# Kernel tuning notes

Measured on AMD Instinct MI355X. Metric: run time of the kernel, lower is better.

Reference implementation:

```python
import jax, jax.numpy as jnp
import numpy as np

PATCH, STRIDE, TOPK, EPS = 16, 8, 8, 1e-8

def _leaky(x):
    return jax.nn.leaky_relu(x, 0.01)

def setup_inputs() -> dict:
    key = jax.random.key(0)
    ks = jax.random.split(key, 12)
    s = 0.05  # small weight scale to avoid tanh saturation
    return {
        "X":      jax.random.normal(ks[0], (16, 4096, 512), jnp.float32),
        "W_enc1": jax.random.normal(ks[1], (512, 256), jnp.float32) * s,
        "b_enc1": jax.random.normal(ks[2], (256,), jnp.float32) * s,
        "W_enc2": jax.random.normal(ks[3], (256, 64), jnp.float32) * s,
        "b_enc2": jax.random.normal(ks[4], (64,), jnp.float32) * s,
        "Wq":     jax.random.normal(ks[5], (64, 64), jnp.float32) * s,
        "Wk":     jax.random.normal(ks[6], (64, 64), jnp.float32) * s,
        "Wv":     jax.random.normal(ks[7], (64, 64), jnp.float32) * s,
        "W_agg":  jax.random.normal(ks[8], (64, 64), jnp.float32) * s,
        "b_agg":  jax.random.normal(ks[9], (64,), jnp.float32) * s,
        "W_dec":  jax.random.normal(ks[10], (64, 512), jnp.float32) * s,
        "b_dec":  jax.random.normal(ks[11], (512,), jnp.float32) * s,
    }

def reference(X, W_enc1, b_enc1, W_enc2, b_enc2, Wq, Wk, Wv, W_agg, b_agg, W_dec, b_dec):
    B, L, D = X.shape
    # var_encoder (dropout-free MLP)
    Xe = _leaky(X @ W_enc1 + b_enc1) @ W_enc2 + b_enc2          # (B, L, d)
    d = Xe.shape[-1]
    # unfold into overlapping patches
    h = (L - PATCH) // STRIDE + 1
    pos = jnp.arange(h)[:, None] * STRIDE + jnp.arange(PATCH)[None, :]  # (h, PATCH)
    patches = Xe[:, pos, :]                                      # (B, h, PATCH, d)
    per_patch = patches.mean(axis=2).reshape(B * h, d)           # (N, d)
    q = per_patch @ Wq
    k = per_patch @ Wk
    v = per_patch @ Wv                                           # (N, hqk)
    qn = q / (jnp.linalg.norm(q, axis=-1, keepdims=True) + EPS)
    kn = k / (jnp.linalg.norm(k, axis=-1, keepdims=True) + EPS)
    # antisymmetric outer product, (N, hqk, hqk)
    M = qn[:, :, None] * kn[:, None, :] - kn[:, :, None] * qn[:, None, :]
    A = jax.nn.relu(jnp.tanh(M))
    n = A.shape[-1]
    # topk pruning along last dim via scatter-style mask
    _, idx = jax.lax.top_k(A, TOPK)                              # (N, n, TOPK)
    mask = jnp.any(idx[..., None] == jnp.arange(n), axis=-2)     # (N, n, n) bool
    A = A * mask.astype(A.dtype)
    A = A / jnp.maximum(A.sum(axis=-1, keepdims=True), EPS)
    Av = jnp.einsum('nij,nj->ni', A, v)                          # (N, hqk)
    # after_agg (dropout = identity in eval)
    z = _leaky(Av @ W_agg + b_agg)                               # (N, d)
    zB = z.reshape(B, h, d)
    # overlap-add fold: each patch writes its (constant-over-time) z to its window
    seg = jnp.broadcast_to(zB[:, :, None, :], (B, h, PATCH, d)).reshape(B, h * PATCH, d)
    flat_pos = pos.reshape(-1)                                   # (h*PATCH,)
    out = jnp.zeros((B, L, d), X.dtype).at[:, flat_pos, :].add(seg)
    counts = jnp.zeros((L,), X.dtype).at[flat_pos].add(1.0)
    out = out / jnp.maximum(counts, 1.0)[None, :, None]
    return out @ W_dec + b_dec                                   # (B, L, D)
```

## Files before the change

### kernel.cpp

```cpp
#include <hip/hip_runtime.h>


typedef __attribute__((ext_vector_type(8))) _Float16 half8;
typedef __attribute__((ext_vector_type(4))) _Float16 half4;
typedef __attribute__((ext_vector_type(4))) float floatx4;

__device__ __forceinline__ _Float16 f2h(float f) { return (_Float16)f; }

#define MFMA16(A, B, C) __builtin_amdgcn_mfma_f32_16x16x32_f16((A), (B), (C), 0, 0, 0)

__global__ __launch_bounds__(256) void prep_weights(
    const float* __restrict__ W1, const float* __restrict__ W2,
    const float* __restrict__ Wd,
    _Float16* __restrict__ W1t, _Float16* __restrict__ W2t,
    _Float16* __restrict__ Wdt)
{
    int idx = blockIdx.x * 256 + threadIdx.x;
    { int n = idx >> 9, k = idx & 511;  W1t[idx] = f2h(W1[k * 256 + n]); }
    if (idx < 16384) { int n = idx >> 8, k = idx & 255; W2t[idx] = f2h(W2[k * 64 + n]); }
    if (idx < 32768) { int n = idx >> 6, k = idx & 63;  Wdt[idx] = f2h(Wd[k * 512 + n]); }
}

__global__ __launch_bounds__(256) void enc_fused(
    const float* __restrict__ X, const _Float16* __restrict__ W1t,
    const float* __restrict__ b1, const _Float16* __restrict__ W2t,
    const float* __restrict__ b2, float* __restrict__ Gs)
{
    __shared__ _Float16 smem[20992];
    _Float16* As   = smem;
    _Float16* Bs   = smem + 4608;
    _Float16* Hs16 = smem;

    const int tid  = threadIdx.x;
    const int lane = tid & 63;
    const int w    = tid >> 6;
    const int m0   = blockIdx.x * 64;

    const int arow  = tid >> 2;
    const int akseg = (tid & 3) << 4;
    const float* Abase = X + (size_t)(m0 + arow) * 512 + akseg;

    const int brow0  = (w << 6) + (lane >> 3);
    const int bchunk = (((lane & 7) ^ ((lane >> 3) & 7)) << 3);

    floatx4 acc1[4][4];
#pragma unroll
    for (int ci = 0; ci < 4; ci++)
#pragma unroll
        for (int mi = 0; mi < 4; mi++) acc1[ci][mi] = (floatx4){0.f, 0.f, 0.f, 0.f};

    float4 pa[4];
    auto loadA = [&](int kt) {
#pragma unroll
        for (int u = 0; u < 4; u++) pa[u] = *(const float4*)(Abase + kt + 4 * u);
    };

    loadA(0);
    for (int kt = 0; kt < 512; kt += 64) {
#pragma unroll
        for (int inst = 0; inst < 8; inst++) {
            const _Float16* src = W1t + (size_t)(brow0 + inst * 8) * 512 + kt + bchunk;
            __builtin_amdgcn_global_load_lds(
                (const __attribute__((address_space(1))) unsigned int*)src,
                (__attribute__((address_space(3))) unsigned int*)(Bs + ((w << 6) + inst * 8) * 64),
                16, 0, 0);
        }
        {
            _Float16* d = &As[arow * 72 + akseg];
#pragma unroll
            for (int h = 0; h < 2; h++) {
                float4 f0 = pa[2 * h], f1 = pa[2 * h + 1];
                half8 o;
                o[0] = f2h(f0.x); o[1] = f2h(f0.y); o[2] = f2h(f0.z); o[3] = f2h(f0.w);
                o[4] = f2h(f1.x); o[5] = f2h(f1.y); o[6] = f2h(f1.z); o[7] = f2h(f1.w);
                *(half8*)(d + 8 * h) = o;
            }
        }
        __syncthreads();
        if (kt + 64 < 512) loadA(kt + 64);
#pragma unroll
        for (int ks = 0; ks < 2; ks++) {
            const int lchunk = ks * 4 + (lane >> 4);
            half8 af[4], bf[4];
#pragma unroll
            for (int ci = 0; ci < 4; ci++) {
                const int c = (w << 6) + ci * 16 + (lane & 15);
                af[ci] = *(const half8*)&Bs[c * 64 + ((lchunk ^ (lane & 7)) << 3)];
            }
#pragma unroll
            for (int mi = 0; mi < 4; mi++)
                bf[mi] = *(const half8*)&As[(mi * 16 + (lane & 15)) * 72 + ks * 32 + ((lane >> 4) << 3)];
#pragma unroll
            for (int ci = 0; ci < 4; ci++)
#pragma unroll
                for (int mi = 0; mi < 4; mi++)
                    acc1[ci][mi] = MFMA16(af[ci], bf[mi], acc1[ci][mi]);
        }
        __syncthreads();
    }

    float4 b1v[4];
#pragma unroll
    for (int ci = 0; ci < 4; ci++)
        b1v[ci] = *(const float4*)&b1[(w << 6) + ci * 16 + ((lane >> 4) << 2)];
#pragma unroll
    for (int ci = 0; ci < 4; ci++) {
#pragma unroll
        for (int mi = 0; mi < 4; mi++) {
            float vs[4];
#pragma unroll
            for (int r = 0; r < 4; r++) {
                float v = acc1[ci][mi][r] + ((const float*)&b1v[ci])[r];
                vs[r] = v > 0.f ? v : 0.01f * v;
            }
#pragma unroll
            for (int r = 0; r < 4; r++) {
                vs[r] += __shfl_xor(vs[r], 1);
                vs[r] += __shfl_xor(vs[r], 2);
                vs[r] += __shfl_xor(vs[r], 4);
            }
            if ((lane & 7) == 0) {
                const int gl = 2 * mi + ((lane & 15) >> 3);
                half4 hv;
#pragma unroll
                for (int r = 0; r < 4; r++) hv[r] = f2h(vs[r]);
                *(half4*)&Hs16[gl * 264 + (w << 6) + ci * 16 + ((lane >> 4) << 2)] = hv;
            }
        }
    }
    __syncthreads();

    floatx4 acc2 = (floatx4){0.f, 0.f, 0.f, 0.f};
    const int kq = (lane >> 4) << 3;
#pragma unroll
    for (int ks = 0; ks < 8; ks++) {
        half8 af = *(const half8*)&Hs16[(lane & 15) * 264 + ks * 32 + kq];
        half8 bf = *(const half8*)&W2t[(size_t)((w << 4) + (lane & 15)) * 256 + ks * 32 + kq];
        acc2 = MFMA16(af, bf, acc2);
    }
    if (lane < 32) {
        const int n = (w << 4) + (lane & 15);
        const float bb = 8.f * b2[n];
        const int gbase = blockIdx.x * 8;
#pragma unroll
        for (int r = 0; r < 4; r++) {
            const int g = ((lane >> 4) << 2) + r;
            Gs[(size_t)(gbase + g) * 64 + n] = acc2[r] + bb;
        }
    }
}

#define TOP8_INS(mv) do { float _x = (mv); float _t;            \
    _t = fmaxf(s0,_x); _x = fminf(s0,_x); s0 = _t;              \
    _t = fmaxf(s1,_x); _x = fminf(s1,_x); s1 = _t;              \
    _t = fmaxf(s2,_x); _x = fminf(s2,_x); s2 = _t;              \
    _t = fmaxf(s3,_x); _x = fminf(s3,_x); s3 = _t;              \
    _t = fmaxf(s4,_x); _x = fminf(s4,_x); s4 = _t;              \
    _t = fmaxf(s5,_x); _x = fminf(s5,_x); s5 = _t;              \
    _t = fmaxf(s6,_x); _x = fminf(s6,_x); s6 = _t;              \
    s7 = fmaxf(s7,_x); } while (0)

__global__ __launch_bounds__(256) void patch_attn(
    const float* __restrict__ Gs,  const float* __restrict__ Wq,
    const float* __restrict__ Wk,  const float* __restrict__ Wv,
    const float* __restrict__ Wagg, const float* __restrict__ bagg,
    float* __restrict__ zout)
{
    __shared__ float sh[4][336];
    const int w    = threadIdx.x >> 6;
    const int lane = threadIdx.x & 63;
    const int n = blockIdx.x * 4 + w;
    const int b = n / 511;
    const int i = n - b * 511;
    float* pp  = &sh[w][0];
    float* qs  = pp + 64;
    float* ksm = pp + 128;
    float* vsm = pp + 192;
    float* avs = pp + 256;

    const float* gp = Gs + ((size_t)(b * 512 + i)) * 64 + lane;
    pp[lane] = (gp[0] + gp[64]) * 0.0625f;
    __syncthreads();

    float q = 0.f, k = 0.f, v = 0.f;
#pragma unroll 4
    for (int e = 0; e < 64; e += 4) {
        float4 p4 = *(const float4*)&pp[e];
        q = fmaf(p4.x, Wq[(e+0)*64+lane], q); q = fmaf(p4.y, Wq[(e+1)*64+lane], q);
        q = fmaf(p4.z, Wq[(e+2)*64+lane], q); q = fmaf(p4.w, Wq[(e+3)*64+lane], q);
        k = fmaf(p4.x, Wk[(e+0)*64+lane], k); k = fmaf(p4.y, Wk[(e+1)*64+lane], k);
        k = fmaf(p4.z, Wk[(e+2)*64+lane], k); k = fmaf(p4.w, Wk[(e+3)*64+lane], k);
        v = fmaf(p4.x, Wv[(e+0)*64+lane], v); v = fmaf(p4.y, Wv[(e+1)*64+lane], v);
        v = fmaf(p4.z, Wv[(e+2)*64+lane], v); v = fmaf(p4.w, Wv[(e+3)*64+lane], v);
    }
    float sq = q * q, sk = k * k;
#pragma unroll
    for (int o = 1; o < 64; o <<= 1) { sq += __shfl_xor(sq, o); sk += __shfl_xor(sk, o); }
    const float qni = q / (sqrtf(sq) + 1e-8f);
    const float kni = k / (sqrtf(sk) + 1e-8f);
    qs[lane] = qni; ksm[lane] = kni; vsm[lane] = v;
    __syncthreads();

    auto MV = [&](float kj, float qj) { return fmaf(qni, kj, -(kni * qj)); };

    float s0=-1e30f,s1=-1e30f,s2=-1e30f,s3=-1e30f,s4=-1e30f,s5=-1e30f,s6=-1e30f,s7=-1e30f;
#pragma unroll
    for (int j = 0; j < 64; j += 4) {
        float4 k4 = *(const float4*)&ksm[j];
        float4 q4 = *(const float4*)&qs[j];
        TOP8_INS(MV(k4.x, q4.x)); TOP8_INS(MV(k4.y, q4.y));
        TOP8_INS(MV(k4.z, q4.z)); TOP8_INS(MV(k4.w, q4.w));
    }
    const float teff = fmaxf(s7, 1e-37f) * (1.f - 1.2e-7f);

    float ssum = 0.f, av = 0.f;
#pragma unroll
    for (int j = 0; j < 64; j += 4) {
        float4 k4 = *(const float4*)&ksm[j];
        float4 q4 = *(const float4*)&qs[j];
        float4 v4 = *(const float4*)&vsm[j];
#define P2(KJ, QJ, VJ) do { float _m = MV(KJ, QJ); float _x2 = _m * _m;           \
        float _a = _m * (15.f + _x2) * __builtin_amdgcn_rcpf(fmaf(6.f, _x2, 15.f)); \
        float _am = (_m >= teff) ? _a : 0.f;                                       \
        ssum += _am; av = fmaf(_am, (VJ), av); } while (0)
        P2(k4.x, q4.x, v4.x); P2(k4.y, q4.y, v4.y);
        P2(k4.z, q4.z, v4.z); P2(k4.w, q4.w, v4.w);
#undef P2
    }
    avs[lane] = av / fmaxf(ssum, 1e-8f);
    __syncthreads();

    float zc = bagg[lane];
#pragma unroll 4
    for (int e = 0; e < 64; e += 4) {
        float4 a4 = *(const float4*)&avs[e];
        zc = fmaf(a4.x, Wagg[(e+0)*64+lane], zc); zc = fmaf(a4.y, Wagg[(e+1)*64+lane], zc);
        zc = fmaf(a4.z, Wagg[(e+2)*64+lane], zc); zc = fmaf(a4.w, Wagg[(e+3)*64+lane], zc);
    }
    zc = zc > 0.f ? zc : 0.01f * zc;
    zout[(size_t)n * 64 + lane] = zc;
}

__global__ __launch_bounds__(256) void dec_fused(
    const float* __restrict__ z, const _Float16* __restrict__ Wdt,
    const float* __restrict__ bd, float* __restrict__ out)
{
    __shared__ _Float16 As[128 * 72];
    __shared__ _Float16 Bs[128 * 72];
    const int tid  = threadIdx.x;
    const int lane = tid & 63;
    const int w    = tid >> 6;
    const int m0 = blockIdx.y * 128, n0 = blockIdx.x * 128;
    const int wrow = (w & 1) << 6, wcol = (w >> 1) << 6;

    {
        const int arow  = tid >> 1;
        const int akseg = (tid & 1) << 5;
        const int row = m0 + arow;
        const int b = row >> 12, l = row & 4095, g = l >> 3;
        const int g0 = g - 1 >= 0 ? g - 1 : 0;
        const int g1 = g <= 510 ? g : 510;
        const float w0 = (g >= 1) ? 1.f : 0.f;
        const float w1 = (g <= 510) ? 1.f : 0.f;
        const float sc = (w0 + w1) > 1.5f ? 0.5f : 1.f;
        const float* z0 = z + ((size_t)(b * 511 + g0)) * 64 + akseg;
        const float* z1 = z + ((size_t)(b * 511 + g1)) * 64 + akseg;
        _Float16* d = &As[arow * 72 + akseg];
#pragma unroll
        for (int u = 0; u < 4; u++) {
            float4 f0a = *(const float4*)(z0 + 8 * u);
            float4 f0b = *(const float4*)(z0 + 8 * u + 4);
            float4 f1a = *(const float4*)(z1 + 8 * u);
            float4 f1b = *(const float4*)(z1 + 8 * u + 4);
            half8 o;
            o[0] = f2h((f0a.x * w0 + f1a.x * w1) * sc);
            o[1] = f2h((f0a.y * w0 + f1a.y * w1) * sc);
            o[2] = f2h((f0a.z * w0 + f1a.z * w1) * sc);
            o[3] = f2h((f0a.w * w0 + f1a.w * w1) * sc);
            o[4] = f2h((f0b.x * w0 + f1b.x * w1) * sc);
            o[5] = f2h((f0b.y * w0 + f1b.y * w1) * sc);
            o[6] = f2h((f0b.z * w0 + f1b.z * w1) * sc);
            o[7] = f2h((f0b.w * w0 + f1b.w * w1) * sc);
            *(half8*)(d + 8 * u) = o;
        }
    }
    {
        const int brow  = tid >> 1;
        const int bkseg = (tid & 1) << 5;
        const _Float16* s = Wdt + (size_t)(n0 + brow) * 64 + bkseg;
        _Float16* d = &Bs[brow * 72 + bkseg];
#pragma unroll
        for (int u = 0; u < 4; u++) *(half8*)(d + 8 * u) = *(const half8*)(s + 8 * u);
    }
    __syncthreads();

    floatx4 accf[4][4];
#pragma unroll
    for (int mi = 0; mi < 4; mi++)
#pragma unroll
        for (int ni = 0; ni < 4; ni++) accf[mi][ni] = (floatx4){0.f, 0.f, 0.f, 0.f};
#pragma unroll
    for (int ks = 0; ks < 2; ks++) {
        const int koff = ks * 32 + ((lane >> 4) << 3);
        half8 af[4], bf[4];
#pragma unroll
        for (int mi = 0; mi < 4; mi++)
            af[mi] = *(const half8*)&As[(wrow + mi * 16 + (lane & 15)) * 72 + koff];
#pragma unroll
        for (int ni = 0; ni < 4; ni++)
            bf[ni] = *(const half8*)&Bs[(wcol + ni * 16 + (lane & 15)) * 72 + koff];
#pragma unroll
        for (int mi = 0; mi < 4; mi++)
#pragma unroll
            for (int ni = 0; ni < 4; ni++)
                accf[mi][ni] = MFMA16(af[mi], bf[ni], accf[mi][ni]);
    }

    float bvv[4];
#pragma unroll
    for (int ni = 0; ni < 4; ni++) bvv[ni] = bd[n0 + wcol + ni * 16 + (lane & 15)];

    float* Cs = (float*)As;
#pragma unroll
    for (int c = 0; c < 4; c++) {
        __syncthreads();
        const int own_wrow = ((c * 32) / 64) * 64;
        if (wrow == own_wrow) {
#pragma unroll
            for (int mm = 0; mm < 2; mm++) {
                const int mi = ((c * 32) % 64) / 16 + mm;
#pragma unroll
                for (int ni = 0; ni < 4; ni++) {
#pragma unroll
                    for (int r = 0; r < 4; r++) {
                        const int lr  = mm * 16 + ((lane >> 4) << 2) + r;
                        const int col = wcol + ni * 16 + (lane & 15);
                        Cs[lr * 128 + col] = accf[mi][ni][r] + bvv[ni];
                    }
                }
            }
        }
        __syncthreads();
#pragma unroll
        for (int u = 0; u < 4; u++) {
            const int idx = (u * 256 + tid) * 4;
            const int lr = idx >> 7, col = idx & 127;
            float4 vv = *(const float4*)&Cs[idx];
            *(float4*)&out[(size_t)(m0 + c * 32 + lr) * 512 + n0 + col] = vv;
        }
    }
}

extern "C" void kernel_launch(void* const* d_in, const int* in_sizes, int n_in,
                              void* d_out, int out_size, void* d_ws, size_t ws_size,
                              hipStream_t stream)
{
    const float* X    = (const float*)d_in[0];
    const float* W1   = (const float*)d_in[1];
    const float* b1   = (const float*)d_in[2];
    const float* W2   = (const float*)d_in[3];
    const float* b2   = (const float*)d_in[4];
    const float* Wq   = (const float*)d_in[5];
    const float* Wk   = (const float*)d_in[6];
    const float* Wv   = (const float*)d_in[7];
    const float* Wagg = (const float*)d_in[8];
    const float* bagg = (const float*)d_in[9];
    const float* Wd   = (const float*)d_in[10];
    const float* bd   = (const float*)d_in[11];

    char* ws = (char*)d_ws;
    float*    Gs  = (float*)(ws);
    float*    z   = (float*)(ws + 2097152);
    _Float16* W1t = (_Float16*)(ws + 4194304);
    _Float16* W2t = (_Float16*)(ws + 4456448);
    _Float16* Wdt = (_Float16*)(ws + 4489216);
    float* out = (float*)d_out;

    prep_weights<<<512, 256, 0, stream>>>(W1, W2, Wd, W1t, W2t, Wdt);
    enc_fused<<<1024, 256, 0, stream>>>(X, W1t, b1, W2t, b2, Gs);
    patch_attn<<<2044, 256, 0, stream>>>(Gs, Wq, Wk, Wv, Wagg, bagg, z);
    dec_fused<<<dim3(4, 512), 256, 0, stream>>>(z, Wdt, bd, out);
}
```

Before: 317.4 us.

## Load encoder GEMM operands directly from global memory into registers, dropping LDS staging

The first encoder GEMM stops staging X and W1t tiles through shared memory with barriers and instead has each wave load its MFMA fragments straight from global memory (X converted to fp16 in registers). Shared memory shrinks to only the hidden buffer, and the per-tile syncthreads go away, which is meant to improve occupancy and cut LDS and barrier overhead. The cost is that each wave re-reads the whole X tile from global/L2 (4x redundancy across waves), and loads are strided per lane with no explicit prefetch pipelining.

```diff
diff --git a/kernel.cpp b/kernel.cpp
--- a/kernel.cpp
+++ b/kernel.cpp
@@ -26,22 +26,16 @@
     const float* __restrict__ b1, const _Float16* __restrict__ W2t,
     const float* __restrict__ b2, float* __restrict__ Gs)
 {
-    __shared__ _Float16 smem[20992];
-    _Float16* As   = smem;
-    _Float16* Bs   = smem + 4608;
-    _Float16* Hs16 = smem;
-
+    __shared__ _Float16 Hs16[16 * 264];
     const int tid  = threadIdx.x;
     const int lane = tid & 63;
     const int w    = tid >> 6;
     const int m0   = blockIdx.x * 64;
-
-    const int arow  = tid >> 2;
-    const int akseg = (tid & 3) << 4;
-    const float* Abase = X + (size_t)(m0 + arow) * 512 + akseg;
-
-    const int brow0  = (w << 6) + (lane >> 3);
-    const int bchunk = (((lane & 7) ^ ((lane >> 3) & 7)) << 3);
+    const int mr   = lane & 15;
+    const int kq   = (lane >> 4) << 3;
+
+    const float*    Xp = X   + (size_t)(m0 + mr) * 512 + kq;
+    const _Float16* Wp = W1t + (size_t)((w << 6) + mr) * 512 + kq;
 
     floatx4 acc1[4][4];
 #pragma unroll
@@ -49,54 +43,31 @@
 #pragma unroll
         for (int mi = 0; mi < 4; mi++) acc1[ci][mi] = (floatx4){0.f, 0.f, 0.f, 0.f};
 
-    float4 pa[4];
-    auto loadA = [&](int kt) {
-#pragma unroll
-        for (int u = 0; u < 4; u++) pa[u] = *(const float4*)(Abase + kt + 4 * u);
-    };
-
-    loadA(0);
-    for (int kt = 0; kt < 512; kt += 64) {
-#pragma unroll
-        for (int inst = 0; inst < 8; inst++) {
-            const _Float16* src = W1t + (size_t)(brow0 + inst * 8) * 512 + kt + bchunk;
-            __builtin_amdgcn_global_load_lds(
-                (const __attribute__((address_space(1))) unsigned int*)src,
-                (__attribute__((address_space(3))) unsigned int*)(Bs + ((w << 6) + inst * 8) * 64),
-                16, 0, 0);
-        }
-        {
-            _Float16* d = &As[arow * 72 + akseg];
-#pragma unroll
-            for (int h = 0; h < 2; h++) {
-                float4 f0 = pa[2 * h], f1 = pa[2 * h + 1];
+#pragma unroll
+    for (int t = 0; t < 8; t++) {
+#pragma unroll
+        for (int ks = 0; ks < 2; ks++) {
+            const int ko = t * 64 + ks * 32;
+            half8 af[4];
+#pragma unroll
+            for (int ci = 0; ci < 4; ci++)
+                af[ci] = *(const half8*)(Wp + (size_t)ci * (16 * 512) + ko);
+            half8 bf[4];
+#pragma unroll
+            for (int mi = 0; mi < 4; mi++) {
+                float4 f0 = *(const float4*)(Xp + (size_t)mi * (16 * 512) + ko);
+                float4 f1 = *(const float4*)(Xp + (size_t)mi * (16 * 512) + ko + 4);
                 half8 o;
                 o[0] = f2h(f0.x); o[1] = f2h(f0.y); o[2] = f2h(f0.z); o[3] = f2h(f0.w);
                 o[4] = f2h(f1.x); o[5] = f2h(f1.y); o[6] = f2h(f1.z); o[7] = f2h(f1.w);
-                *(half8*)(d + 8 * h) = o;
-            }
-        }
-        __syncthreads();
-        if (kt + 64 < 512) loadA(kt + 64);
-#pragma unroll
-        for (int ks = 0; ks < 2; ks++) {
-            const int lchunk = ks * 4 + (lane >> 4);
-            half8 af[4], bf[4];
-#pragma unroll
-            for (int ci = 0; ci < 4; ci++) {
-                const int c = (w << 6) + ci * 16 + (lane & 15);
-                af[ci] = *(const half8*)&Bs[c * 64 + ((lchunk ^ (lane & 7)) << 3)];
-            }
-#pragma unroll
-            for (int mi = 0; mi < 4; mi++)
-                bf[mi] = *(const half8*)&As[(mi * 16 + (lane & 15)) * 72 + ks * 32 + ((lane >> 4) << 3)];
+                bf[mi] = o;
+            }
 #pragma unroll
             for (int ci = 0; ci < 4; ci++)
 #pragma unroll
                 for (int mi = 0; mi < 4; mi++)
                     acc1[ci][mi] = MFMA16(af[ci], bf[mi], acc1[ci][mi]);
         }
-        __syncthreads();
     }
 
     float4 b1v[4];
@@ -131,7 +102,6 @@
     __syncthreads();
 
     floatx4 acc2 = (floatx4){0.f, 0.f, 0.f, 0.f};
-    const int kq = (lane >> 4) << 3;
 #pragma unroll
     for (int ks = 0; ks < 8; ks++) {
         half8 af = *(const half8*)&Hs16[(lane & 15) * 264 + ks * 32 + kq];
```

After: 361.1 us. +13.8%, slower.
